# Kernel optimization log

Measured on AMD Instinct MI355X. Metric: run time of the kernel, lower is better.

Reference implementation:

```python
import jax, jax.numpy as jnp
import numpy as np

T, B = 2048, 16384  # sequence_length, minibatch_size

def setup_inputs() -> dict:
    key = jax.random.key(0)
    ks = jax.random.split(key, 6)
    return {
        "x": jax.random.normal(ks[0], (T, B, 1), dtype=jnp.float32),
        "W1": jax.random.normal(ks[1], (4, 2), dtype=jnp.float32) * 0.5,
        "W2": jax.random.normal(ks[2], (4, 4), dtype=jnp.float32) * 0.5,
        "b2": jax.random.normal(ks[3], (4,), dtype=jnp.float32) * 0.1,
        "W3": jax.random.normal(ks[4], (4, 4), dtype=jnp.float32) * 0.5,
        "W4": jax.random.normal(ks[5], (1, 4), dtype=jnp.float32) * 0.5,
    }

def reference(x, W1, b2, W2, W3, W4):
    # x: (T, B, 1). State starts at zeros (self.state is None -> zeros), no teacher forcing.
    def step(state, x_t):
        # state: (B, 1); x_t: (B, 1)
        inp = jnp.concatenate([x_t, state], axis=-1)        # (B, 2)
        h = jnp.tanh(inp @ W1.T)                            # (B, 4)
        h = jnp.tanh(h @ W2.T + b2)                         # (B, 4)
        h = jnp.tanh(h @ W3.T)                              # (B, 4)
        d = h @ W4.T                                        # (B, 1)
        out = d + state                                     # residual state feedback
        return out, out
    state0 = jnp.zeros((x.shape[1], 1), dtype=x.dtype)
    _, outs = jax.lax.scan(step, state0, x)                 # outs: (T, B, 1)
    return outs
```

## Files before the change

kernel.cpp:

```cpp
#include <hip/hip_runtime.h>

#define TT 2048

__device__ __forceinline__ float tanh_pre(float z) {
    float t = __builtin_amdgcn_exp2f(z);
    float r = __builtin_amdgcn_rcpf(1.0f + t);
    return fmaf(-2.0f, r, 1.0f);
}

template<int CTRL>
__device__ __forceinline__ float dpp_f(float x) {
    return __int_as_float(__builtin_amdgcn_mov_dpp(__float_as_int(x), CTRL, 0xf, 0xf, true));
}
#define QP_ROT1 0x39
#define QP_ROT2 0x4E
#define QP_ROT3 0x93
#define QP_XOR1 0xB1

__global__ __launch_bounds__(256, 1)
void stn_quad_kernel(const float* __restrict__ x,
                     const float* __restrict__ W1,
                     const float* __restrict__ W2,
                     const float* __restrict__ b2,
                     const float* __restrict__ W3,
                     const float* __restrict__ W4,
                     float* __restrict__ out, int B)
{
    const int tid = blockIdx.x * blockDim.x + threadIdx.x;
    const int q   = tid & 3;
    const int b   = tid >> 2;
    if (b >= B) return;
    const float K = 2.8853900817779268f;

    const float w1x = W1[q*2+0] * K;
    const float w1s = W1[q*2+1] * K;
    const float bb  = b2[q] * K;
    const float w4l = W4[q];
    float w2q[4], w3q[4];
    #pragma unroll
    for (int r = 0; r < 4; ++r) {
        w2q[r] = W2[q*4 + ((q+r)&3)] * K;
        w3q[r] = W3[q*4 + ((q+r)&3)] * K;
    }

    const float* xp = x + b;
    float* op = out + b;
    float s = 0.0f;

    constexpr int U = 4;
    float xb[U];
    #pragma unroll
    for (int k = 0; k < U; ++k) xb[k] = __builtin_nontemporal_load(xp + k*B);
    xp += (size_t)U * B;

    for (int t = 0; t < TT; t += U) {
        float xc[U];
        #pragma unroll
        for (int k = 0; k < U; ++k) xc[k] = xb[k];
        if (t + U < TT) {
            #pragma unroll
            for (int k = 0; k < U; ++k) xb[k] = __builtin_nontemporal_load(xp + k*B);
        }
        xp += (size_t)U * B;

        #pragma unroll
        for (int k = 0; k < U; ++k) {
            float h1 = tanh_pre(fmaf(w1s, s, w1x * xc[k]));

            float h1r1 = dpp_f<QP_ROT1>(h1);
            float h1r2 = dpp_f<QP_ROT2>(h1);
            float h1r3 = dpp_f<QP_ROT3>(h1);
            float a2 = bb;
            a2 = fmaf(w2q[0], h1,   a2);
            a2 = fmaf(w2q[1], h1r1, a2);
            a2 = fmaf(w2q[2], h1r2, a2);
            a2 = fmaf(w2q[3], h1r3, a2);
            float h2 = tanh_pre(a2);

            float h2r1 = dpp_f<QP_ROT1>(h2);
            float h2r2 = dpp_f<QP_ROT2>(h2);
            float h2r3 = dpp_f<QP_ROT3>(h2);
            float a3 = w3q[0] * h2;
            a3 = fmaf(w3q[1], h2r1, a3);
            a3 = fmaf(w3q[2], h2r2, a3);
            a3 = fmaf(w3q[3], h2r3, a3);
            float h3 = tanh_pre(a3);

            float p = w4l * h3;
            p += dpp_f<QP_XOR1>(p);
            p += dpp_f<QP_ROT2>(p);
            s += p;

            if (q == 0) __builtin_nontemporal_store(s, op);
            op += B;
        }
    }
}

extern "C" void kernel_launch(void* const* d_in, const int* in_sizes, int n_in,
                              void* d_out, int out_size, void* d_ws, size_t ws_size,
                              hipStream_t stream)
{
    const float* x  = (const float*)d_in[0];
    const float* W1 = (const float*)d_in[1];
    const float* A2 = (const float*)d_in[2];
    const float* A3 = (const float*)d_in[3];
    const float* W3 = (const float*)d_in[4];
    const float* W4 = (const float*)d_in[5];
    const float* W2 = (in_sizes[2] == 16) ? A2 : A3;
    const float* b2 = (in_sizes[2] == 16) ? A3 : A2;

    const int B = in_sizes[0] / TT;
    float* out = (float*)d_out;

    const int threads = B * 4;
    dim3 block(256);
    dim3 grid((threads + 255) / 256);
    hipLaunchKernelGGL(stn_quad_kernel, grid, block, 0, stream,
                       x, W1, W2, b2, W3, W4, out, B);
}
```

Measured before the change: 429.1 us.

## Fold tanh affine terms into weights and use 8 lanes per batch element

Rewrites tanh(z)=1-2*sigma(-2z) so each layer evaluates only rcp(1+exp2) and folds the constant offsets into precomputed biases (B2, B3, C4). This shortens the serial dependency chain per timestep. It also precomputes the next step's input term off the critical path and spreads each batch element over 8 lanes, so each lane writes one output out of every 8 timesteps instead of lane 0 doing all stores. The cost is twice as many threads, with all 8 lanes doing redundant compute per element, and more register pressure from the 8-deep input buffers.

```diff
diff --git a/kernel.cpp b/kernel.cpp
--- a/kernel.cpp
+++ b/kernel.cpp
@@ -1,12 +1,6 @@
 #include <hip/hip_runtime.h>
 
 #define TT 2048
-
-__device__ __forceinline__ float tanh_pre(float z) {
-    float t = __builtin_amdgcn_exp2f(z);
-    float r = __builtin_amdgcn_rcpf(1.0f + t);
-    return fmaf(-2.0f, r, 1.0f);
-}
 
 template<int CTRL>
 __device__ __forceinline__ float dpp_f(float x) {
@@ -15,84 +9,106 @@
 #define QP_ROT1 0x39
 #define QP_ROT2 0x4E
 #define QP_ROT3 0x93
-#define QP_XOR1 0xB1
 
-__global__ __launch_bounds__(256, 1)
-void stn_quad_kernel(const float* __restrict__ x,
-                     const float* __restrict__ W1,
-                     const float* __restrict__ W2,
-                     const float* __restrict__ b2,
-                     const float* __restrict__ W3,
-                     const float* __restrict__ W4,
-                     float* __restrict__ out, int B)
+__device__ __forceinline__ float sigma_r(float z) {
+    return __builtin_amdgcn_rcpf(1.0f + __builtin_amdgcn_exp2f(z));
+}
+
+__global__ __launch_bounds__(512, 2)
+void stn_oct_kernel(const float* __restrict__ x,
+                    const float* __restrict__ W1,
+                    const float* __restrict__ W2,
+                    const float* __restrict__ b2,
+                    const float* __restrict__ W3,
+                    const float* __restrict__ W4,
+                    float* __restrict__ out, int B)
 {
     const int tid = blockIdx.x * blockDim.x + threadIdx.x;
-    const int q   = tid & 3;
-    const int b   = tid >> 2;
+    const int o   = tid & 7;
+    const int q   = o & 3;
+    const int b   = tid >> 3;
     if (b >= B) return;
     const float K = 2.8853900817779268f;
 
-    const float w1x = W1[q*2+0] * K;
-    const float w1s = W1[q*2+1] * K;
-    const float bb  = b2[q] * K;
-    const float w4l = W4[q];
-    float w2q[4], w3q[4];
+    const float Kw1x = W1[2*q]   * K;
+    const float Kw1s = W1[2*q+1] * K;
+    float B2 = b2[q], B3 = 0.f, C4 = 0.f;
+    float a2[4], a3[4], a4[4];
     #pragma unroll
     for (int r = 0; r < 4; ++r) {
-        w2q[r] = W2[q*4 + ((q+r)&3)] * K;
-        w3q[r] = W3[q*4 + ((q+r)&3)] * K;
+        const int j = (q + r) & 3;
+        a2[r] = -2.f * K * W2[q*4 + j];
+        a3[r] = -2.f * K * W3[q*4 + j];
+        a4[r] = -2.f * W4[j];
+        B2 += W2[q*4 + r];
+        B3 += W3[q*4 + r];
+        C4 += W4[r];
     }
+    B2 *= K; B3 *= K;
 
     const float* xp = x + b;
-    float* op = out + b;
-    float s = 0.0f;
+    float* op = out + b + (size_t)o * B;
 
-    constexpr int U = 4;
-    float xb[U];
+    float cur[8], nxt[8];
     #pragma unroll
-    for (int k = 0; k < U; ++k) xb[k] = __builtin_nontemporal_load(xp + k*B);
-    xp += (size_t)U * B;
+    for (int j = 0; j < 8; ++j) cur[j] = __builtin_nontemporal_load(xp + j*B);
+    #pragma unroll
+    for (int j = 0; j < 8; ++j) nxt[j] = __builtin_nontemporal_load(xp + (8+j)*B);
 
-    for (int t = 0; t < TT; t += U) {
-        float xc[U];
+    float psum = 0.f;
+    float sC   = C4;
+    float pre2 = Kw1x * cur[0];
+
+    for (int t = 0; t < TT; t += 8) {
+        float outv[8];
         #pragma unroll
-        for (int k = 0; k < U; ++k) xc[k] = xb[k];
-        if (t + U < TT) {
+        for (int k = 0; k < 8; ++k) {
+            float z1 = fmaf(Kw1s, psum, pre2);
+            float r1 = sigma_r(z1);
+            float xn = (k < 7) ? cur[k+1] : nxt[0];
+            pre2 = fmaf(Kw1s, sC, Kw1x * xn);
+            float rA = dpp_f<QP_ROT1>(r1);
+            float rB = dpp_f<QP_ROT2>(r1);
+            float rC = dpp_f<QP_ROT3>(r1);
+            float m0 = fmaf(a2[0], r1, B2);
+            float u1 = fmaf(a2[1], rA, m0);
+            float v  = a2[2] * rB;
+            float u2 = fmaf(a2[3], rC, v);
+            float r2 = sigma_r(u1 + u2);
+            rA = dpp_f<QP_ROT1>(r2);
+            rB = dpp_f<QP_ROT2>(r2);
+            rC = dpp_f<QP_ROT3>(r2);
+            m0 = fmaf(a3[0], r2, B3);
+            u1 = fmaf(a3[1], rA, m0);
+            v  = a3[2] * rB;
+            u2 = fmaf(a3[3], rC, v);
+            float r3 = sigma_r(u1 + u2);
+            rA = dpp_f<QP_ROT1>(r3);
+            rB = dpp_f<QP_ROT2>(r3);
+            rC = dpp_f<QP_ROT3>(r3);
+            float p0 = a4[0] * r3;
+            u1 = fmaf(a4[1], rA, p0);
+            v  = a4[2] * rB;
+            u2 = fmaf(a4[3], rC, v);
+            psum = u1 + u2;
+            outv[k] = sC + psum;
+            sC = outv[k] + C4;
+        }
+        float s01 = (o & 1) ? outv[1] : outv[0];
+        float s23 = (o & 1) ? outv[3] : outv[2];
+        float s45 = (o & 1) ? outv[5] : outv[4];
+        float s67 = (o & 1) ? outv[7] : outv[6];
+        float sA  = (o & 2) ? s23 : s01;
+        float sB  = (o & 2) ? s67 : s45;
+        float sv  = (o & 4) ? sB  : sA;
+        __builtin_nontemporal_store(sv, op);
+        op += (size_t)8 * B;
+        #pragma unroll
+        for (int j = 0; j < 8; ++j) cur[j] = nxt[j];
+        if (t + 16 < TT) {
             #pragma unroll
-            for (int k = 0; k < U; ++k) xb[k] = __builtin_nontemporal_load(xp + k*B);
-        }
-        xp += (size_t)U * B;
-
-        #pragma unroll
-        for (int k = 0; k < U; ++k) {
-            float h1 = tanh_pre(fmaf(w1s, s, w1x * xc[k]));
-
-            float h1r1 = dpp_f<QP_ROT1>(h1);
-            float h1r2 = dpp_f<QP_ROT2>(h1);
-            float h1r3 = dpp_f<QP_ROT3>(h1);
-            float a2 = bb;
-            a2 = fmaf(w2q[0], h1,   a2);
-            a2 = fmaf(w2q[1], h1r1, a2);
-            a2 = fmaf(w2q[2], h1r2, a2);
-            a2 = fmaf(w2q[3], h1r3, a2);
-            float h2 = tanh_pre(a2);
-
-            float h2r1 = dpp_f<QP_ROT1>(h2);
-            float h2r2 = dpp_f<QP_ROT2>(h2);
-            float h2r3 = dpp_f<QP_ROT3>(h2);
-            float a3 = w3q[0] * h2;
-            a3 = fmaf(w3q[1], h2r1, a3);
-            a3 = fmaf(w3q[2], h2r2, a3);
-            a3 = fmaf(w3q[3], h2r3, a3);
-            float h3 = tanh_pre(a3);
-
-            float p = w4l * h3;
-            p += dpp_f<QP_XOR1>(p);
-            p += dpp_f<QP_ROT2>(p);
-            s += p;
-
-            if (q == 0) __builtin_nontemporal_store(s, op);
-            op += B;
+            for (int j = 0; j < 8; ++j)
+                nxt[j] = __builtin_nontemporal_load(xp + (size_t)(t+16+j)*B);
         }
     }
 }
@@ -113,9 +129,9 @@
     const int B = in_sizes[0] / TT;
     float* out = (float*)d_out;
 
-    const int threads = B * 4;
-    dim3 block(256);
-    dim3 grid((threads + 255) / 256);
-    hipLaunchKernelGGL(stn_quad_kernel, grid, block, 0, stream,
+    const int threads = B * 8;
+    dim3 block(512);
+    dim3 grid((threads + 511) / 512);
+    hipLaunchKernelGGL(stn_oct_kernel, grid, block, 0, stream,
                        x, W1, W2, b2, W3, W4, out, B);
 }
```

New measurement: 390.3 us, median of 2. 1.1x faster.
